# Optimization experiments

Hardware: AMD Instinct MI355X
Metric: run time of the kernel (lower is better)

Reference implementation:

```python
import jax, jax.numpy as jnp
import numpy as np

N, E, F_IN, HID, EMB = 100000, 3200000, 128, 16, 8
NEG_SLOPE = 0.2


def _seg_softmax(logits, seg, n):
    # Numerically stable softmax over segments (per trailing channel if 2D).
    m = jax.ops.segment_max(logits, seg, num_segments=n)
    e = jnp.exp(logits - m[seg])
    s = jax.ops.segment_sum(e, seg, num_segments=n)
    return e / s[seg]


def _gatv2(x, src, dst, Wl, Wr, att, bias, t, n):
    # GATv2Conv, heads=1, add_self_loops=False, eval mode (dropout off),
    # with learnable SoftmaxAggregation replacing the sum aggregation.
    xl = x @ Wl                      # [N, C] source transform
    xr = x @ Wr                      # [N, C] target transform
    score = jnp.sum(jax.nn.leaky_relu(xl[src] + xr[dst], NEG_SLOPE) * att, axis=-1)  # [E]
    alpha = _seg_softmax(score, dst, n)          # attention softmax over incoming edges
    m = xl[src] * alpha[:, None]                 # [E, C] messages
    w = _seg_softmax(m * t, dst, n)              # SoftmaxAggregation(learn=True), per channel
    return jax.ops.segment_sum(w * m, dst, num_segments=n) + bias


def setup_inputs() -> dict:
    key = jax.random.key(0)
    ks = iter(jax.random.split(key, 32))
    r = lambda shape, s=0.1: jax.random.normal(next(ks), shape, dtype=jnp.float32) * s
    return dict(
        x=r((N, F_IN), 1.0),
        edge_index=jax.random.randint(next(ks), (2, E), 0, N, dtype=jnp.int32),
        batch=jnp.arange(N, dtype=jnp.int32),
        Wl1=r((F_IN, HID)), Wr1=r((F_IN, HID)), att1=r((HID,)), b1=r((HID,)),
        Wlin1=r((F_IN, HID)), blin1=r((HID,)),
        Wl2=r((HID, EMB)), Wr2=r((HID, EMB)), att2=r((EMB,)), b2=r((EMB,)),
        Wlin2=r((HID, EMB)), blin2=r((EMB,)),
        t=jnp.ones((1,), jnp.float32),
        W3=r((EMB, EMB)), b3=r((EMB,)),
        W4=r((EMB, 1)), b4=r((1,)),
        W5=r((1, 1)), b5=r((1,)),
        Wout=r((1, 1)), bout=r((1,)),
    )


def reference(x, edge_index, batch, Wl1, Wr1, att1, b1, Wlin1, blin1,
              Wl2, Wr2, att2, b2, Wlin2, blin2, t,
              W3, b3, W4, b4, W5, b5, Wout, bout):
    n = x.shape[0]
    src, dst = edge_index[0], edge_index[1]
    # layer 1: GATv2 + skip Linear, relu, global_add_pool
    h = _gatv2(x, src, dst, Wl1, Wr1, att1, b1, t, n) + (x @ Wlin1 + blin1)
    h = jax.nn.relu(h)
    g = jax.ops.segment_sum(h, batch, num_segments=n)  # global_add_pool (batch=arange(N))
    # layer 2: GATv2 + skip Linear on pooled tensor (as in original code), relu, pool
    h2 = _gatv2(g, src, dst, Wl2, Wr2, att2, b2, t, n) + (g @ Wlin2 + blin2)
    h2 = jax.nn.relu(h2)
    g2 = jax.ops.segment_sum(h2, batch, num_segments=n)
    # small MLP head
    z = jax.nn.relu(g2 @ W3 + b3)
    z = jax.nn.relu(z @ W4 + b4)
    z = jax.nn.relu(z @ W5 + b5)
    return jax.nn.log_sigmoid(z @ Wout + bout)
```

## Files before the change

### kernel.cpp

```cpp
#include <hip/hip_runtime.h>
#include <hip/hip_bf16.h>
#include <math.h>

#define F_IN 128
#define C1 16
#define C2 8

#define LBITS 8
#define LOCAL (1 << LBITS)
#define NB_MAX 512
#define ITEMS 16

static __device__ __forceinline__ unsigned short f2bf(float f) {
  __hip_bfloat16 h = __float2bfloat16(f);
  return *(unsigned short*)&h;
}

__global__ void bucket_hist(const int* __restrict__ dst, int* __restrict__ bcount, int E, int NB) {
  __shared__ int h[NB_MAX];
  for (int i = threadIdx.x; i < NB; i += blockDim.x) h[i] = 0;
  __syncthreads();
  int stride = gridDim.x * blockDim.x;
  for (int e = blockIdx.x * blockDim.x + threadIdx.x; e < E; e += stride)
    atomicAdd(&h[dst[e] >> LBITS], 1);
  __syncthreads();
  for (int i = threadIdx.x; i < NB; i += blockDim.x)
    if (h[i]) atomicAdd(&bcount[i], h[i]);
}

__global__ void bucket_scan(const int* __restrict__ bcount, int* __restrict__ bbase,
                            int* __restrict__ bcursor, int NB) {
  __shared__ int sd[NB_MAX];
  int t = threadIdx.x;
  int v = (t < NB) ? bcount[t] : 0;
  sd[t] = v;
  __syncthreads();
  int acc = v;
  for (int off = 1; off < NB_MAX; off <<= 1) {
    int u = (t >= off) ? sd[t - off] : 0;
    __syncthreads();
    acc += u;
    sd[t] = acc;
    __syncthreads();
  }
  if (t < NB) {
    int excl = acc - v;
    bbase[t] = excl;
    bcursor[t] = excl;
    if (t == NB - 1) bbase[NB] = acc;
  }
}

__global__ void phaseA_lds(const int* __restrict__ src, const int* __restrict__ dst,
                           int* __restrict__ bcursor, int* __restrict__ packed, int E, int NB) {
  __shared__ int hist[NB_MAX];
  __shared__ int cur[NB_MAX];
  for (int i = threadIdx.x; i < NB; i += blockDim.x) hist[i] = 0;
  __syncthreads();
  int base = blockIdx.x * blockDim.x * ITEMS;
  int vals[ITEMS];
  int bkt[ITEMS];
#pragma unroll
  for (int k = 0; k < ITEMS; k++) {
    int e = base + k * blockDim.x + threadIdx.x;
    if (e < E) {
      int s = src[e];
      int d = dst[e];
      bkt[k] = d >> LBITS;
      vals[k] = (s << LBITS) | (d & (LOCAL - 1));
      atomicAdd(&hist[bkt[k]], 1);
    } else {
      bkt[k] = -1;
    }
  }
  __syncthreads();
  for (int i = threadIdx.x; i < NB; i += blockDim.x) {
    int c = hist[i];
    cur[i] = c ? atomicAdd(&bcursor[i], c) : 0;
  }
  __syncthreads();
#pragma unroll
  for (int k = 0; k < ITEMS; k++) {
    if (bkt[k] >= 0) {
      int p = atomicAdd(&cur[bkt[k]], 1);
      packed[p] = vals[k];
    }
  }
}

__global__ void phaseB_sort(const int* __restrict__ packed, const int* __restrict__ bbase,
                            int* __restrict__ row_ptr, int* __restrict__ ssrc, int N, int E) {
  __shared__ int h[LOCAL];
  __shared__ int sd[LOCAL];
  int b = blockIdx.x;
  int t = threadIdx.x;
  int beg = bbase[b], end = bbase[b + 1];
  int node0 = b << LBITS;
  h[t] = 0;
  __syncthreads();
  for (int j = beg + t; j < end; j += blockDim.x) atomicAdd(&h[packed[j] & (LOCAL - 1)], 1);
  __syncthreads();
  int cnt = h[t];
  sd[t] = cnt;
  __syncthreads();
  int acc = cnt;
  for (int off = 1; off < LOCAL; off <<= 1) {
    int u = (t >= off) ? sd[t - off] : 0;
    __syncthreads();
    acc += u;
    sd[t] = acc;
    __syncthreads();
  }
  int myex = acc - cnt;
  int node = node0 + t;
  if (node < N) row_ptr[node] = beg + myex;
  h[t] = beg + myex;
  if (b == gridDim.x - 1 && t == 0) row_ptr[N] = E;
  __syncthreads();
  for (int j = beg + t; j < end; j += blockDim.x) {
    int v = packed[j];
    int p = atomicAdd(&h[v & (LOCAL - 1)], 1);
    ssrc[p] = v >> LBITS;
  }
}

__global__ __launch_bounds__(256) void gemm3_128x16(
    const float* __restrict__ x, const float* __restrict__ Wl, const float* __restrict__ Wr,
    const float* __restrict__ Wlin, const float* __restrict__ blin,
    __hip_bfloat16* __restrict__ XLh, float* __restrict__ XR, float* __restrict__ SK, int N) {
  int bx = blockIdx.x;
  int mat = bx % 3;
  int node = (bx / 3) * 256 + threadIdx.x;
  if (node >= N) return;
  const float* __restrict__ W = (mat == 0) ? Wl : (mat == 1) ? Wr : Wlin;
  const float4* xr4 = (const float4*)(x + (size_t)node * F_IN);
  float acc[16];
#pragma unroll
  for (int c = 0; c < 16; c++) acc[c] = 0.f;
#pragma unroll 8
  for (int kk = 0; kk < F_IN / 4; kk++) {
    float4 xv = xr4[kk];
    float xs[4] = {xv.x, xv.y, xv.z, xv.w};
#pragma unroll
    for (int j = 0; j < 4; j++) {
      int k = kk * 4 + j;
#pragma unroll
      for (int c = 0; c < 16; c++) acc[c] = fmaf(xs[j], W[k * 16 + c], acc[c]);
    }
  }
  if (mat == 0) {
    unsigned int pk[8];
#pragma unroll
    for (int i = 0; i < 8; i++)
      pk[i] = (unsigned)f2bf(acc[2 * i]) | ((unsigned)f2bf(acc[2 * i + 1]) << 16);
    uint4* xlp = (uint4*)(XLh + (size_t)node * 16);
    xlp[0] = make_uint4(pk[0], pk[1], pk[2], pk[3]);
    xlp[1] = make_uint4(pk[4], pk[5], pk[6], pk[7]);
  } else if (mat == 1) {
    float4* xrp = (float4*)(XR + (size_t)node * 16);
#pragma unroll
    for (int q = 0; q < 4; q++)
      xrp[q] = make_float4(acc[4 * q], acc[4 * q + 1], acc[4 * q + 2], acc[4 * q + 3]);
  } else {
    float4* skp = (float4*)(SK + (size_t)node * 16);
#pragma unroll
    for (int q = 0; q < 4; q++)
      skp[q] = make_float4(acc[4 * q] + blin[4 * q], acc[4 * q + 1] + blin[4 * q + 1],
                           acc[4 * q + 2] + blin[4 * q + 2], acc[4 * q + 3] + blin[4 * q + 3]);
  }
}

__global__ __launch_bounds__(256) void gemm3_16x8(
    const float* __restrict__ Hin, const float* __restrict__ Wl, const float* __restrict__ Wr,
    const float* __restrict__ Wlin, const float* __restrict__ blin,
    __hip_bfloat16* __restrict__ XLh, float* __restrict__ XR, float* __restrict__ SK, int N) {
  int bx = blockIdx.x;
  int mat = bx % 3;
  int node = (bx / 3) * 256 + threadIdx.x;
  if (node >= N) return;
  const float* __restrict__ W = (mat == 0) ? Wl : (mat == 1) ? Wr : Wlin;
  const float4* hr4 = (const float4*)(Hin + (size_t)node * 16);
  float acc[8];
#pragma unroll
  for (int c = 0; c < 8; c++) acc[c] = 0.f;
#pragma unroll
  for (int kk = 0; kk < 4; kk++) {
    float4 hv = hr4[kk];
    float hs[4] = {hv.x, hv.y, hv.z, hv.w};
#pragma unroll
    for (int j = 0; j < 4; j++) {
      int k = kk * 4 + j;
#pragma unroll
      for (int c = 0; c < 8; c++) acc[c] = fmaf(hs[j], W[k * 8 + c], acc[c]);
    }
  }
  if (mat == 0) {
    unsigned int pk[4];
#pragma unroll
    for (int i = 0; i < 4; i++)
      pk[i] = (unsigned)f2bf(acc[2 * i]) | ((unsigned)f2bf(acc[2 * i + 1]) << 16);
    *(uint4*)(XLh + (size_t)node * 8) = make_uint4(pk[0], pk[1], pk[2], pk[3]);
  } else if (mat == 1) {
    float4* xrp = (float4*)(XR + (size_t)node * 8);
#pragma unroll
    for (int q = 0; q < 2; q++)
      xrp[q] = make_float4(acc[4 * q], acc[4 * q + 1], acc[4 * q + 2], acc[4 * q + 3]);
  } else {
    float4* skp = (float4*)(SK + (size_t)node * 8);
#pragma unroll
    for (int q = 0; q < 2; q++)
      skp[q] = make_float4(acc[4 * q] + blin[4 * q], acc[4 * q + 1] + blin[4 * q + 1],
                           acc[4 * q + 2] + blin[4 * q + 2], acc[4 * q + 3] + blin[4 * q + 3]);
  }
}

template <int C, int POOL, bool HEAD>
__global__ __launch_bounds__(256) void gat_layer(
    const __hip_bfloat16* __restrict__ XLh, const float* __restrict__ XR,
    const float* __restrict__ SK, const float* __restrict__ att, const float* __restrict__ bias,
    const float* __restrict__ tp, const int* __restrict__ row_ptr, const int* __restrict__ ssrc,
    float* __restrict__ H, int N,
    const float* __restrict__ W3, const float* __restrict__ b3, const float* __restrict__ W4,
    const float* __restrict__ b4, const float* __restrict__ W5, const float* __restrict__ b5,
    const float* __restrict__ Wout, const float* __restrict__ bout, float* __restrict__ out) {
  constexpr int NPB = 256 / C;
  constexpr int LOGNPB = (NPB == 16) ? 4 : 5;
  __shared__ __align__(16) unsigned short vpool[POOL * C];
  __shared__ float ppool[POOL];
  __shared__ __align__(16) float xrl[NPB * C];
  __shared__ float invS0s[NPB];
  __shared__ int nb[NPB + 1];
  __shared__ float hsh[HEAD ? NPB * C : 1];
  int t = threadIdx.x;
  int node0 = blockIdx.x * NPB;

  if (t <= NPB) {
    int nd = node0 + t;
    nb[t] = row_ptr[(nd < N) ? nd : N];
  }
  {
    size_t xi = (size_t)node0 * C + t;
    xrl[t] = (xi < (size_t)N * C) ? XR[xi] : 0.f;
  }
  float attr[C];
#pragma unroll
  for (int cc = 0; cc < C; cc++) attr[cc] = att[cc];
  float tval = tp[0];
  __syncthreads();

  int bbeg = nb[0];
  int nE = nb[NPB] - bbeg;
  int nCap = (nE < POOL) ? nE : POOL;
  const unsigned short* XLu = (const unsigned short*)XLh;

  for (int slot = t; slot < nCap; slot += 256) {
    int sb = slot + bbeg;
    int lo = 0, hi = NPB;
#pragma unroll
    for (int st = 0; st < LOGNPB; st++) {
      int mid = (lo + hi) >> 1;
      bool go = nb[mid] <= sb;
      lo = go ? mid : lo;
      hi = go ? hi : mid;
    }
    int g = lo;
    int s = ssrc[sb];
    float v[C];
    if constexpr (C == 16) {
      const uint4* gp = (const uint4*)(XLu + (size_t)s * 16);
      uint4 a = gp[0], b = gp[1];
      *(uint4*)&vpool[slot * 16] = a;
      *(uint4*)&vpool[slot * 16 + 8] = b;
      unsigned arr[8] = {a.x, a.y, a.z, a.w, b.x, b.y, b.z, b.w};
#pragma unroll
      for (int i = 0; i < 8; i++) {
        v[2 * i] = __uint_as_float(arr[i] << 16);
        v[2 * i + 1] = __uint_as_float(arr[i] & 0xffff0000u);
      }
    } else {
      const uint4* gp = (const uint4*)(XLu + (size_t)s * 8);
      uint4 a = gp[0];
      *(uint4*)&vpool[slot * 8] = a;
      unsigned arr[4] = {a.x, a.y, a.z, a.w};
#pragma unroll
      for (int i = 0; i < 4; i++) {
        v[2 * i] = __uint_as_float(arr[i] << 16);
        v[2 * i + 1] = __uint_as_float(arr[i] & 0xffff0000u);
      }
    }
    float xr[C];
    const float4* xp = (const float4*)&xrl[g * C];
#pragma unroll
    for (int q = 0; q < C / 4; q++) {
      float4 f = xp[q];
      xr[4 * q] = f.x;
      xr[4 * q + 1] = f.y;
      xr[4 * q + 2] = f.z;
      xr[4 * q + 3] = f.w;
    }
    float p0 = 0.f, p1 = 0.f, p2 = 0.f, p3 = 0.f;
#pragma unroll
    for (int cc = 0; cc < C; cc += 4) {
      float u0 = v[cc] + xr[cc];
      float u1 = v[cc + 1] + xr[cc + 1];
      float u2 = v[cc + 2] + xr[cc + 2];
      float u3 = v[cc + 3] + xr[cc + 3];
      p0 = fmaf(fmaxf(u0, 0.2f * u0), attr[cc], p0);
      p1 = fmaf(fmaxf(u1, 0.2f * u1), attr[cc + 1], p1);
      p2 = fmaf(fmaxf(u2, 0.2f * u2), attr[cc + 2], p2);
      p3 = fmaf(fmaxf(u3, 0.2f * u3), attr[cc + 3], p3);
    }
    ppool[slot] = __expf((p0 + p1) + (p2 + p3));
  }
  __syncthreads();

  int g = t / C;
  int c = t % C;
  int base = nb[g] - bbeg;
  int deg = nb[g + 1] - nb[g];
  int capd = POOL - base;
  capd = capd < 0 ? 0 : (capd > deg ? deg : capd);

  {
    float s0 = 0.f;
    for (int j = c; j < capd; j += C) s0 += ppool[base + j];
    for (int j = capd + c; j < deg; j += C) {
      int s = ssrc[bbeg + base + j];
      float sc = 0.f;
#pragma unroll
      for (int cc = 0; cc < C; cc++) {
        float v = __bfloat162float(XLh[(size_t)s * C + cc]);
        float u = v + xrl[g * C + cc];
        sc = fmaf(fmaxf(u, 0.2f * u), attr[cc], sc);
      }
      s0 += __expf(sc);
    }
#pragma unroll
    for (int m = 1; m < C; m <<= 1) s0 += __shfl_xor(s0, m, C);
    if (c == 0) invS0s[g] = (deg > 0) ? 1.0f / s0 : 0.f;
  }
  __syncthreads();

  float invS0 = invS0s[g];
  float S1 = 0.f, S2 = 0.f, S1b = 0.f, S2b = 0.f;
  int jj = 0;
  for (; jj + 2 <= capd; jj += 2) {
    int sl0 = base + jj;
    float v0 = __uint_as_float(((unsigned)vpool[sl0 * C + c]) << 16);
    float p0 = ppool[sl0];
    float v1 = __uint_as_float(((unsigned)vpool[(sl0 + 1) * C + c]) << 16);
    float p1 = ppool[sl0 + 1];
    float m0 = v0 * (p0 * invS0);
    float m1 = v1 * (p1 * invS0);
    float w0 = __expf(m0 * tval);
    float w1 = __expf(m1 * tval);
    S1 += w0;
    S2 = fmaf(w0, m0, S2);
    S1b += w1;
    S2b = fmaf(w1, m1, S2b);
  }
  for (; jj < capd; jj++) {
    int sl = base + jj;
    float v = __uint_as_float(((unsigned)vpool[sl * C + c]) << 16);
    float p = ppool[sl];
    float mm = v * (p * invS0);
    float w = __expf(mm * tval);
    S1 += w;
    S2 = fmaf(w, mm, S2);
  }
  for (; jj < deg; jj++) {
    int s = ssrc[bbeg + base + jj];
    float sc = 0.f, vc = 0.f;
#pragma unroll
    for (int cc = 0; cc < C; cc++) {
      float v = __bfloat162float(XLh[(size_t)s * C + cc]);
      if (cc == c) vc = v;
      float u = v + xrl[g * C + cc];
      sc = fmaf(fmaxf(u, 0.2f * u), attr[cc], sc);
    }
    float p = __expf(sc);
    float mm = vc * (p * invS0);
    float w = __expf(mm * tval);
    S1 += w;
    S2 = fmaf(w, mm, S2);
  }
  S1 += S1b;
  S2 += S2b;

  int node = node0 + g;
  bool valid = node < N;
  float hval = 0.f;
  if (valid) {
    float gat = (deg > 0) ? (S2 / S1) : 0.f;
    hval = fmaxf(gat + bias[c] + SK[(size_t)node * C + c], 0.f);
  }
  if constexpr (!HEAD) {
    if (valid) H[(size_t)node * C + c] = hval;
  } else {
    hsh[g * C + c] = hval;
    __syncthreads();
    if (t < NPB) {
      int nd = node0 + t;
      if (nd < N) {
        float h[8];
#pragma unroll
        for (int k = 0; k < 8; k++) h[k] = hsh[t * 8 + k];
        float s4 = 0.f;
#pragma unroll
        for (int cc = 0; cc < 8; cc++) {
          float z = b3[cc];
#pragma unroll
          for (int k = 0; k < 8; k++) z = fmaf(h[k], W3[k * 8 + cc], z);
          z = fmaxf(z, 0.f);
          s4 = fmaf(z, W4[cc], s4);
        }
        s4 = fmaxf(s4 + b4[0], 0.f);
        float s5 = fmaxf(fmaf(s4, W5[0], b5[0]), 0.f);
        float zo = fmaf(s5, Wout[0], bout[0]);
        float ls;
        if (zo >= 0.f)
          ls = -log1pf(expf(-zo));
        else
          ls = zo - log1pf(expf(zo));
        out[nd] = ls;
      }
    }
  }
}

extern "C" void kernel_launch(void* const* d_in, const int* in_sizes, int n_in,
                              void* d_out, int out_size, void* d_ws, size_t ws_size,
                              hipStream_t stream) {
  const float* x = (const float*)d_in[0];
  const int* ei = (const int*)d_in[1];
  const float* Wl1 = (const float*)d_in[3];
  const float* Wr1 = (const float*)d_in[4];
  const float* att1 = (const float*)d_in[5];
  const float* b1 = (const float*)d_in[6];
  const float* Wlin1 = (const float*)d_in[7];
  const float* blin1 = (const float*)d_in[8];
  const float* Wl2 = (const float*)d_in[9];
  const float* Wr2 = (const float*)d_in[10];
  const float* att2 = (const float*)d_in[11];
  const float* b2 = (const float*)d_in[12];
  const float* Wlin2 = (const float*)d_in[13];
  const float* blin2 = (const float*)d_in[14];
  const float* t = (const float*)d_in[15];
  const float* W3 = (const float*)d_in[16];
  const float* b3 = (const float*)d_in[17];
  const float* W4 = (const float*)d_in[18];
  const float* b4 = (const float*)d_in[19];
  const float* W5 = (const float*)d_in[20];
  const float* b5 = (const float*)d_in[21];
  const float* Wout = (const float*)d_in[22];
  const float* bout = (const float*)d_in[23];
  float* out = (float*)d_out;

  int N = in_sizes[0] / F_IN;
  int E = in_sizes[1] / 2;
  const int* src = ei;
  const int* dst = ei + E;
  int NB = (N + LOCAL - 1) >> LBITS;

  char* ws = (char*)d_ws;
  size_t off = 0;
  auto alloc = [&](size_t bytes) -> void* {
    void* p = ws + off;
    off = (off + bytes + 255) & ~(size_t)255;
    return p;
  };
  int* bcount = (int*)alloc((size_t)NB * 4);
  int* bbase = (int*)alloc((size_t)(NB + 1) * 4);
  int* bcursor = (int*)alloc((size_t)NB * 4);
  int* packed = (int*)alloc((size_t)E * 4);
  int* row_ptr = (int*)alloc((size_t)(N + 1) * 4);
  int* ssrc = (int*)alloc((size_t)E * 4);
  __hip_bfloat16* XL1 = (__hip_bfloat16*)alloc((size_t)N * C1 * 2);
  float* XR1 = (float*)alloc((size_t)N * C1 * 4);
  float* SK1 = (float*)alloc((size_t)N * C1 * 4);
  float* H1 = (float*)alloc((size_t)N * C1 * 4);
  __hip_bfloat16* XL2 = (__hip_bfloat16*)alloc((size_t)N * C2 * 2);
  float* XR2 = (float*)alloc((size_t)N * C2 * 4);
  float* SK2 = (float*)alloc((size_t)N * C2 * 4);

  int nblkA = (E + 256 * ITEMS - 1) / (256 * ITEMS);
  int nodeBlk = (N + 255) / 256;

  hipMemsetAsync(bcount, 0, (size_t)NB * 4, stream);
  hipLaunchKernelGGL(bucket_hist, dim3(512), dim3(256), 0, stream, dst, bcount, E, NB);
  hipLaunchKernelGGL(bucket_scan, dim3(1), dim3(NB_MAX), 0, stream, bcount, bbase, bcursor, NB);
  hipLaunchKernelGGL(phaseA_lds, dim3(nblkA), dim3(256), 0, stream, src, dst, bcursor, packed, E,
                     NB);
  hipLaunchKernelGGL(phaseB_sort, dim3(NB), dim3(LOCAL), 0, stream, packed, bbase, row_ptr, ssrc, N,
                     E);
  hipLaunchKernelGGL(gemm3_128x16, dim3(nodeBlk * 3), dim3(256), 0, stream, x, Wl1, Wr1,
                     Wlin1, blin1, XL1, XR1, SK1, N);
  hipLaunchKernelGGL((gat_layer<16, 640, false>), dim3((N + 15) / 16), dim3(256), 0, stream, XL1,
                     XR1, SK1, att1, b1, t, row_ptr, ssrc, H1, N, nullptr, nullptr, nullptr,
                     nullptr, nullptr, nullptr, nullptr, nullptr, nullptr);
  hipLaunchKernelGGL(gemm3_16x8, dim3(nodeBlk * 3), dim3(256), 0, stream, H1, Wl2, Wr2,
                     Wlin2, blin2, XL2, XR2, SK2, N);
  hipLaunchKernelGGL((gat_layer<8, 1280, true>), dim3((N + 31) / 32), dim3(256), 0, stream, XL2,
                     XR2, SK2, att2, b2, t, row_ptr, ssrc, nullptr, N, W3, b3, W4, b4, W5, b5, Wout,
                     bout, out);
}
```

Baseline: 319.9 us.

## Fuse layer-2 projections into layer-1 GAT epilogue and stage bucket scatter in LDS

The layer-1 GAT kernel now computes the three 16x8 projections (Wl2, Wr2, Wlin2 plus bias) in its epilogue from LDS-held node outputs. This removes the separate gemm3_16x8 launch and the H1 round trip through global memory. Separately, phaseA_lds now scans the per-block bucket histogram, stages edges in LDS sorted by bucket, and writes them out with contiguous per-bucket runs, which should coalesce the packed scatter. The cost is more shared memory per phaseA block (about 24KB), which may lower occupancy, plus extra syncs in the GAT epilogue.

```diff
diff --git a/kernel.cpp b/kernel.cpp
--- a/kernel.cpp
+++ b/kernel.cpp
@@ -10,6 +10,7 @@
 #define LOCAL (1 << LBITS)
 #define NB_MAX 512
 #define ITEMS 16
+#define EPB (256 * ITEMS)
 
 static __device__ __forceinline__ unsigned short f2bf(float f) {
   __hip_bfloat16 h = __float2bfloat16(f);
@@ -51,18 +52,25 @@
   }
 }
 
-__global__ void phaseA_lds(const int* __restrict__ src, const int* __restrict__ dst,
-                           int* __restrict__ bcursor, int* __restrict__ packed, int E, int NB) {
+__global__ __launch_bounds__(256) void phaseA_lds(const int* __restrict__ src,
+                                                  const int* __restrict__ dst,
+                                                  int* __restrict__ bcursor,
+                                                  int* __restrict__ packed, int E, int NB) {
   __shared__ int hist[NB_MAX];
-  __shared__ int cur[NB_MAX];
-  for (int i = threadIdx.x; i < NB; i += blockDim.x) hist[i] = 0;
-  __syncthreads();
-  int base = blockIdx.x * blockDim.x * ITEMS;
+  __shared__ int lbase[NB_MAX];
+  __shared__ int gbase[NB_MAX];
+  __shared__ int sdata[256];
+  __shared__ int stage[EPB];
+  __shared__ unsigned short stageb[EPB];
+  int t = threadIdx.x;
+  for (int i = t; i < NB; i += 256) hist[i] = 0;
+  __syncthreads();
+  int base = blockIdx.x * EPB;
   int vals[ITEMS];
   int bkt[ITEMS];
 #pragma unroll
   for (int k = 0; k < ITEMS; k++) {
-    int e = base + k * blockDim.x + threadIdx.x;
+    int e = base + k * 256 + t;
     if (e < E) {
       int s = src[e];
       int d = dst[e];
@@ -74,17 +82,44 @@
     }
   }
   __syncthreads();
-  for (int i = threadIdx.x; i < NB; i += blockDim.x) {
+  int i0 = 2 * t, i1 = 2 * t + 1;
+  int h0 = (i0 < NB) ? hist[i0] : 0;
+  int h1 = (i1 < NB) ? hist[i1] : 0;
+  int s2 = h0 + h1;
+  sdata[t] = s2;
+  __syncthreads();
+  int acc = s2;
+  for (int off = 1; off < 256; off <<= 1) {
+    int u = (t >= off) ? sdata[t - off] : 0;
+    __syncthreads();
+    acc += u;
+    sdata[t] = acc;
+    __syncthreads();
+  }
+  int excl = acc - s2;
+  if (i0 < NB) lbase[i0] = excl;
+  if (i1 < NB) lbase[i1] = excl + h0;
+  __syncthreads();
+  for (int i = t; i < NB; i += 256) {
     int c = hist[i];
-    cur[i] = c ? atomicAdd(&bcursor[i], c) : 0;
+    gbase[i] = c ? atomicAdd(&bcursor[i], c) : 0;
+    hist[i] = lbase[i];
   }
   __syncthreads();
 #pragma unroll
   for (int k = 0; k < ITEMS; k++) {
     if (bkt[k] >= 0) {
-      int p = atomicAdd(&cur[bkt[k]], 1);
-      packed[p] = vals[k];
-    }
+      int lp = atomicAdd(&hist[bkt[k]], 1);
+      stage[lp] = vals[k];
+      stageb[lp] = (unsigned short)bkt[k];
+    }
+  }
+  __syncthreads();
+  int blockE = E - base;
+  if (blockE > EPB) blockE = EPB;
+  for (int i = t; i < blockE; i += 256) {
+    int b = stageb[i];
+    packed[gbase[b] + (i - lbase[b])] = stage[i];
   }
 }
 
@@ -170,59 +205,17 @@
   }
 }
 
-__global__ __launch_bounds__(256) void gemm3_16x8(
-    const float* __restrict__ Hin, const float* __restrict__ Wl, const float* __restrict__ Wr,
-    const float* __restrict__ Wlin, const float* __restrict__ blin,
-    __hip_bfloat16* __restrict__ XLh, float* __restrict__ XR, float* __restrict__ SK, int N) {
-  int bx = blockIdx.x;
-  int mat = bx % 3;
-  int node = (bx / 3) * 256 + threadIdx.x;
-  if (node >= N) return;
-  const float* __restrict__ W = (mat == 0) ? Wl : (mat == 1) ? Wr : Wlin;
-  const float4* hr4 = (const float4*)(Hin + (size_t)node * 16);
-  float acc[8];
-#pragma unroll
-  for (int c = 0; c < 8; c++) acc[c] = 0.f;
-#pragma unroll
-  for (int kk = 0; kk < 4; kk++) {
-    float4 hv = hr4[kk];
-    float hs[4] = {hv.x, hv.y, hv.z, hv.w};
-#pragma unroll
-    for (int j = 0; j < 4; j++) {
-      int k = kk * 4 + j;
-#pragma unroll
-      for (int c = 0; c < 8; c++) acc[c] = fmaf(hs[j], W[k * 8 + c], acc[c]);
-    }
-  }
-  if (mat == 0) {
-    unsigned int pk[4];
-#pragma unroll
-    for (int i = 0; i < 4; i++)
-      pk[i] = (unsigned)f2bf(acc[2 * i]) | ((unsigned)f2bf(acc[2 * i + 1]) << 16);
-    *(uint4*)(XLh + (size_t)node * 8) = make_uint4(pk[0], pk[1], pk[2], pk[3]);
-  } else if (mat == 1) {
-    float4* xrp = (float4*)(XR + (size_t)node * 8);
-#pragma unroll
-    for (int q = 0; q < 2; q++)
-      xrp[q] = make_float4(acc[4 * q], acc[4 * q + 1], acc[4 * q + 2], acc[4 * q + 3]);
-  } else {
-    float4* skp = (float4*)(SK + (size_t)node * 8);
-#pragma unroll
-    for (int q = 0; q < 2; q++)
-      skp[q] = make_float4(acc[4 * q] + blin[4 * q], acc[4 * q + 1] + blin[4 * q + 1],
-                           acc[4 * q + 2] + blin[4 * q + 2], acc[4 * q + 3] + blin[4 * q + 3]);
-  }
-}
-
-template <int C, int POOL, bool HEAD>
+template <int C, int POOL, bool HEAD, bool FUSEG2>
 __global__ __launch_bounds__(256) void gat_layer(
     const __hip_bfloat16* __restrict__ XLh, const float* __restrict__ XR,
     const float* __restrict__ SK, const float* __restrict__ att, const float* __restrict__ bias,
     const float* __restrict__ tp, const int* __restrict__ row_ptr, const int* __restrict__ ssrc,
     float* __restrict__ H, int N,
-    const float* __restrict__ W3, const float* __restrict__ b3, const float* __restrict__ W4,
-    const float* __restrict__ b4, const float* __restrict__ W5, const float* __restrict__ b5,
-    const float* __restrict__ Wout, const float* __restrict__ bout, float* __restrict__ out) {
+    const float* __restrict__ P0, const float* __restrict__ P1, const float* __restrict__ P2,
+    const float* __restrict__ P3, const float* __restrict__ P4, const float* __restrict__ P5,
+    const float* __restrict__ P6, const float* __restrict__ P7,
+    __hip_bfloat16* __restrict__ XL2h, float* __restrict__ XR2, float* __restrict__ SK2,
+    float* __restrict__ out) {
   constexpr int NPB = 256 / C;
   constexpr int LOGNPB = (NPB == 16) ? 4 : 5;
   __shared__ __align__(16) unsigned short vpool[POOL * C];
@@ -230,7 +223,8 @@
   __shared__ __align__(16) float xrl[NPB * C];
   __shared__ float invS0s[NPB];
   __shared__ int nb[NPB + 1];
-  __shared__ float hsh[HEAD ? NPB * C : 1];
+  __shared__ float hsh[(HEAD || FUSEG2) ? NPB * C : 1];
+  __shared__ float wfuse[FUSEG2 ? 392 : 1];
   int t = threadIdx.x;
   int node0 = blockIdx.x * NPB;
 
@@ -241,6 +235,10 @@
   {
     size_t xi = (size_t)node0 * C + t;
     xrl[t] = (xi < (size_t)N * C) ? XR[xi] : 0.f;
+  }
+  if constexpr (FUSEG2) {
+    for (int i = t; i < 392; i += 256)
+      wfuse[i] = (i < 128) ? P0[i] : (i < 256) ? P1[i - 128] : (i < 384) ? P2[i - 256] : P3[i - 384];
   }
   float attr[C];
 #pragma unroll
@@ -394,9 +392,27 @@
     float gat = (deg > 0) ? (S2 / S1) : 0.f;
     hval = fmaxf(gat + bias[c] + SK[(size_t)node * C + c], 0.f);
   }
-  if constexpr (!HEAD) {
-    if (valid) H[(size_t)node * C + c] = hval;
-  } else {
+  if constexpr (FUSEG2) {
+    hsh[g * C + c] = hval;
+    __syncthreads();
+    if (t < NPB * 8) {
+      int g2 = t >> 3, c2 = t & 7;
+      int nd = node0 + g2;
+      if (nd < N) {
+        float a0 = 0.f, a1 = 0.f, a2 = 0.f;
+#pragma unroll
+        for (int k = 0; k < 16; k++) {
+          float hv = hsh[g2 * 16 + k];
+          a0 = fmaf(hv, wfuse[k * 8 + c2], a0);
+          a1 = fmaf(hv, wfuse[128 + k * 8 + c2], a1);
+          a2 = fmaf(hv, wfuse[256 + k * 8 + c2], a2);
+        }
+        ((unsigned short*)XL2h)[(size_t)nd * 8 + c2] = f2bf(a0);
+        XR2[(size_t)nd * 8 + c2] = a1;
+        SK2[(size_t)nd * 8 + c2] = a2 + wfuse[384 + c2];
+      }
+    }
+  } else if constexpr (HEAD) {
     hsh[g * C + c] = hval;
     __syncthreads();
     if (t < NPB) {
@@ -408,15 +424,15 @@
         float s4 = 0.f;
 #pragma unroll
         for (int cc = 0; cc < 8; cc++) {
-          float z = b3[cc];
-#pragma unroll
-          for (int k = 0; k < 8; k++) z = fmaf(h[k], W3[k * 8 + cc], z);
+          float z = P1[cc];
+#pragma unroll
+          for (int k = 0; k < 8; k++) z = fmaf(h[k], P0[k * 8 + cc], z);
           z = fmaxf(z, 0.f);
-          s4 = fmaf(z, W4[cc], s4);
+          s4 = fmaf(z, P2[cc], s4);
         }
-        s4 = fmaxf(s4 + b4[0], 0.f);
-        float s5 = fmaxf(fmaf(s4, W5[0], b5[0]), 0.f);
-        float zo = fmaf(s5, Wout[0], bout[0]);
+        s4 = fmaxf(s4 + P3[0], 0.f);
+        float s5 = fmaxf(fmaf(s4, P4[0], P5[0]), 0.f);
+        float zo = fmaf(s5, P6[0], P7[0]);
         float ls;
         if (zo >= 0.f)
           ls = -log1pf(expf(-zo));
@@ -425,6 +441,8 @@
         out[nd] = ls;
       }
     }
+  } else {
+    if (valid) H[(size_t)node * C + c] = hval;
   }
 }
 
@@ -478,12 +496,11 @@
   __hip_bfloat16* XL1 = (__hip_bfloat16*)alloc((size_t)N * C1 * 2);
   float* XR1 = (float*)alloc((size_t)N * C1 * 4);
   float* SK1 = (float*)alloc((size_t)N * C1 * 4);
-  float* H1 = (float*)alloc((size_t)N * C1 * 4);
   __hip_bfloat16* XL2 = (__hip_bfloat16*)alloc((size_t)N * C2 * 2);
   float* XR2 = (float*)alloc((size_t)N * C2 * 4);
   float* SK2 = (float*)alloc((size_t)N * C2 * 4);
 
-  int nblkA = (E + 256 * ITEMS - 1) / (256 * ITEMS);
+  int nblkA = (E + EPB - 1) / EPB;
   int nodeBlk = (N + 255) / 256;
 
   hipMemsetAsync(bcount, 0, (size_t)NB * 4, stream);
@@ -495,12 +512,10 @@
                      E);
   hipLaunchKernelGGL(gemm3_128x16, dim3(nodeBlk * 3), dim3(256), 0, stream, x, Wl1, Wr1,
                      Wlin1, blin1, XL1, XR1, SK1, N);
-  hipLaunchKernelGGL((gat_layer<16, 640, false>), dim3((N + 15) / 16), dim3(256), 0, stream, XL1,
-                     XR1, SK1, att1, b1, t, row_ptr, ssrc, H1, N, nullptr, nullptr, nullptr,
-                     nullptr, nullptr, nullptr, nullptr, nullptr, nullptr);
-  hipLaunchKernelGGL(gemm3_16x8, dim3(nodeBlk * 3), dim3(256), 0, stream, H1, Wl2, Wr2,
-                     Wlin2, blin2, XL2, XR2, SK2, N);
-  hipLaunchKernelGGL((gat_layer<8, 1280, true>), dim3((N + 31) / 32), dim3(256), 0, stream, XL2,
-                     XR2, SK2, att2, b2, t, row_ptr, ssrc, nullptr, N, W3, b3, W4, b4, W5, b5, Wout,
-                     bout, out);
-}
+  hipLaunchKernelGGL((gat_layer<16, 640, false, true>), dim3((N + 15) / 16), dim3(256), 0, stream,
+                     XL1, XR1, SK1, att1, b1, t, row_ptr, ssrc, nullptr, N, Wl2, Wr2, Wlin2, blin2,
+                     nullptr, nullptr, nullptr, nullptr, XL2, XR2, SK2, nullptr);
+  hipLaunchKernelGGL((gat_layer<8, 1280, true, false>), dim3((N + 31) / 32), dim3(256), 0, stream,
+                     XL2, XR2, SK2, att2, b2, t, row_ptr, ssrc, nullptr, N, W3, b3, W4, b4, W5, b5,
+                     Wout, bout, nullptr, nullptr, nullptr, out);
+}
```

Result: faster. 309.9 us (-3.1%).
